# Kernel tuning notes

Hardware: AMD Instinct MI355X
Metric: run time of the kernel (lower is better)

Reference implementation:

```python
import jax, jax.numpy as jnp
import numpy as np

B, D, N, K = 16, 128, 16384, 64


def setup_inputs() -> dict:
    key = jax.random.key(0)
    k1, k2, k3, k4 = jax.random.split(key, 4)
    x = jax.random.normal(k1, (B, D, N), dtype=jnp.float32)
    mu = jax.random.normal(k2, (K, D), dtype=jnp.float32)
    log_sigma = 0.1 * jax.random.normal(k3, (K, D), dtype=jnp.float32)
    log_alpha = 0.1 * jax.random.normal(k4, (K,), dtype=jnp.float32)
    return {"x": x, "mu": mu, "log_sigma": log_sigma, "log_alpha": log_alpha}


def reference(x, mu, log_sigma, log_alpha):
    # x: (B, D, N) -> (B, N, D)
    xt = jnp.transpose(x, (0, 2, 1))
    # F.normalize(mu): L2-normalize each cluster center along D (eps=1e-12)
    mu_n = mu / jnp.maximum(jnp.linalg.norm(mu, axis=1, keepdims=True), 1e-12)
    sigma_inv = jnp.exp(-log_sigma)                     # (K, D)
    log_sigma_sum = jnp.sum(log_sigma, axis=1)          # (K,)
    # dist_{bnk} = sum_d (x-mu)^2 * sinv, decomposed into GEMMs
    xsq_term = jnp.einsum('bnd,kd->bnk', xt * xt, sigma_inv)
    cross = jnp.einsum('bnd,kd->bnk', xt, mu_n * sigma_inv)
    mu_term = jnp.sum(mu_n * mu_n * sigma_inv, axis=1)  # (K,)
    dist = xsq_term - 2.0 * cross + mu_term
    logits = -dist + log_alpha - 0.5 * log_sigma_sum    # (B, N, K)
    posterior = jax.nn.softmax(logits, axis=-1)
    return jnp.transpose(posterior, (0, 2, 1))          # (B, K, N)
```

## Files before the change

### kernel.cpp

```cpp
#include <hip/hip_runtime.h>

#define LOG2E 1.4426950408889634f

constexpr int Dn = 128;
constexpr int Nn = 16384;
constexpr int Kn = 64;
constexpr int Bn = 16;

typedef __attribute__((ext_vector_type(16))) float f32x16;

__global__ __launch_bounds__(64) void gmm_prep(const float* __restrict__ mu,
                                               const float* __restrict__ log_sigma,
                                               const float* __restrict__ log_alpha,
                                               float4* __restrict__ wout,
                                               float* __restrict__ cout) {
    const int k = blockIdx.x;
    const int l = threadIdx.x;
    const int d0 = 2 * l;
    float m0 = mu[k * Dn + d0];
    float m1 = mu[k * Dn + d0 + 1];
    float s0 = log_sigma[k * Dn + d0];
    float s1 = log_sigma[k * Dn + d0 + 1];
    float nrm2 = m0 * m0 + m1 * m1;
    float lss = s0 + s1;
    #pragma unroll
    for (int off = 32; off > 0; off >>= 1) {
        nrm2 += __shfl_xor(nrm2, off);
        lss  += __shfl_xor(lss, off);
    }
    const float inv_nrm = 1.0f / fmaxf(sqrtf(nrm2), 1e-12f);
    const float mn0 = m0 * inv_nrm, mn1 = m1 * inv_nrm;
    const float si0 = expf(-s0), si1 = expf(-s1);
    float mt = mn0 * mn0 * si0 + mn1 * mn1 * si1;
    #pragma unroll
    for (int off = 32; off > 0; off >>= 1) mt += __shfl_xor(mt, off);
    wout[((k >> 3) * 64 + l) * 8 + (k & 7)] =
        make_float4(-si0 * LOG2E, 2.0f * mn0 * si0 * LOG2E,
                    -si1 * LOG2E, 2.0f * mn1 * si1 * LOG2E);
    if (l == 0) cout[k] = (log_alpha[k] - 0.5f * lss - mt) * LOG2E;
}

__device__ __forceinline__ float4 fmax4(float4 a, float4 b) {
    return make_float4(fmaxf(a.x, b.x), fmaxf(a.y, b.y),
                       fmaxf(a.z, b.z), fmaxf(a.w, b.w));
}
__device__ __forceinline__ float4 add4(float4 a, float4 b) {
    return make_float4(a.x + b.x, a.y + b.y, a.z + b.z, a.w + b.w);
}

__global__ __launch_bounds__(512)
void gmm_main(const float* __restrict__ x,
              const float4* __restrict__ w,
              const float* __restrict__ cks,
              float* __restrict__ out) {
    __shared__ float sRed[8][256];

    const int tid = threadIdx.x;
    const int g = __builtin_amdgcn_readfirstlane(tid >> 6);
    const int l = tid & 63;
    const int b = blockIdx.y;
    const int nloc = 4 * l;
    const size_t nbase = (size_t)blockIdx.x * 256 + nloc;

    float acc[8][4];
    #pragma unroll
    for (int k = 0; k < 8; ++k) {
        const float c = cks[g * 8 + k];
        #pragma unroll
        for (int j = 0; j < 4; ++j) acc[k][j] = c;
    }

    const float* xp = x + (size_t)b * Dn * Nn + nbase;
    const char* wp = (const char*)w + (size_t)g * 8192;

    #pragma unroll 1
    for (int dh = 0; dh < Dn / 2; ++dh) {
        const float4 xa = *(const float4*)(xp);
        const float4 xb = *(const float4*)(xp + Nn);
        xp += 2 * Nn;

        f32x16 w0, w1;
        asm("s_load_dwordx16 %0, %2, 0x0\n\t"
            "s_load_dwordx16 %1, %2, 0x40\n\t"
            "s_waitcnt lgkmcnt(0)"
            : "=&s"(w0), "=&s"(w1)
            : "s"(wp));
        wp += 128;

        const float4 ta = make_float4(xa.x * xa.x, xa.y * xa.y,
                                      xa.z * xa.z, xa.w * xa.w);
        const float4 tb = make_float4(xb.x * xb.x, xb.y * xb.y,
                                      xb.z * xb.z, xb.w * xb.w);

#define GMM_K(WV, KK, A)                                                  \
        {                                                                 \
            const float wx0 = WV[4 * KK + 0], wy0 = WV[4 * KK + 1];       \
            const float wx1 = WV[4 * KK + 2], wy1 = WV[4 * KK + 3];       \
            A[0] = fmaf(wx0, ta.x, A[0]); A[0] = fmaf(wy0, xa.x, A[0]);   \
            A[0] = fmaf(wx1, tb.x, A[0]); A[0] = fmaf(wy1, xb.x, A[0]);   \
            A[1] = fmaf(wx0, ta.y, A[1]); A[1] = fmaf(wy0, xa.y, A[1]);   \
            A[1] = fmaf(wx1, tb.y, A[1]); A[1] = fmaf(wy1, xb.y, A[1]);   \
            A[2] = fmaf(wx0, ta.z, A[2]); A[2] = fmaf(wy0, xa.z, A[2]);   \
            A[2] = fmaf(wx1, tb.z, A[2]); A[2] = fmaf(wy1, xb.z, A[2]);   \
            A[3] = fmaf(wx0, ta.w, A[3]); A[3] = fmaf(wy0, xa.w, A[3]);   \
            A[3] = fmaf(wx1, tb.w, A[3]); A[3] = fmaf(wy1, xb.w, A[3]);   \
        }

        GMM_K(w0, 0, acc[0]); GMM_K(w0, 1, acc[1]);
        GMM_K(w0, 2, acc[2]); GMM_K(w0, 3, acc[3]);
        GMM_K(w1, 0, acc[4]); GMM_K(w1, 1, acc[5]);
        GMM_K(w1, 2, acc[6]); GMM_K(w1, 3, acc[7]);
#undef GMM_K
    }

    float4 m = make_float4(acc[0][0], acc[0][1], acc[0][2], acc[0][3]);
    #pragma unroll
    for (int k = 1; k < 8; ++k)
        m = fmax4(m, make_float4(acc[k][0], acc[k][1], acc[k][2], acc[k][3]));
    *(float4*)&sRed[g][nloc] = m;
    __syncthreads();
    #pragma unroll
    for (int gg = 0; gg < 8; ++gg)
        m = fmax4(m, *(const float4*)&sRed[gg][nloc]);
    __syncthreads();

    float4 s = make_float4(0.f, 0.f, 0.f, 0.f);
    #pragma unroll
    for (int k = 0; k < 8; ++k) {
        acc[k][0] = __builtin_amdgcn_exp2f(acc[k][0] - m.x); s.x += acc[k][0];
        acc[k][1] = __builtin_amdgcn_exp2f(acc[k][1] - m.y); s.y += acc[k][1];
        acc[k][2] = __builtin_amdgcn_exp2f(acc[k][2] - m.z); s.z += acc[k][2];
        acc[k][3] = __builtin_amdgcn_exp2f(acc[k][3] - m.w); s.w += acc[k][3];
    }
    *(float4*)&sRed[g][nloc] = s;
    __syncthreads();
    s = make_float4(0.f, 0.f, 0.f, 0.f);
    #pragma unroll
    for (int gg = 0; gg < 8; ++gg)
        s = add4(s, *(const float4*)&sRed[gg][nloc]);
    const float4 r = make_float4(1.0f / s.x, 1.0f / s.y, 1.0f / s.z, 1.0f / s.w);

    float* op = out + (size_t)(b * Kn + g * 8) * Nn + nbase;
    #pragma unroll
    for (int k = 0; k < 8; ++k) {
        *(float4*)op = make_float4(acc[k][0] * r.x, acc[k][1] * r.y,
                                   acc[k][2] * r.z, acc[k][3] * r.w);
        op += Nn;
    }
}

extern "C" void kernel_launch(void* const* d_in, const int* in_sizes, int n_in,
                              void* d_out, int out_size, void* d_ws, size_t ws_size,
                              hipStream_t stream) {
    const float* x  = (const float*)d_in[0];
    const float* mu = (const float*)d_in[1];
    const float* ls = (const float*)d_in[2];
    const float* la = (const float*)d_in[3];
    float* out = (float*)d_out;

    float4* wbuf = (float4*)d_ws;
    float*  cbuf = (float*)((char*)d_ws + (size_t)Kn * (Dn / 2) * sizeof(float4));

    gmm_prep<<<dim3(Kn), dim3(64), 0, stream>>>(mu, ls, la, wbuf, cbuf);
    gmm_main<<<dim3(Nn / 256, Bn), dim3(512), 0, stream>>>(x, wbuf, cbuf, out);
}
```

Before: 261.5 us.

## Split clusters across 16 waves per block and software-prefetch x rows

Each block now runs 16 waves of 64 lanes, each handling 4 clusters instead of 8, so the same 256 points are covered by twice as many waves. The weight layout in the prep kernel changes to match, and the cross-wave softmax reduction grows to 16 rows. The main loop now handles four d-rows per iteration and prefetches the next four x rows into registers while computing the current ones, using a safe dummy address on the last iteration. This aims to raise occupancy and hide global-load latency, at the cost of every wave reading x redundantly (16 times per block instead of 8) and a larger shared-memory reduction.

```diff
diff --git a/kernel.cpp b/kernel.cpp
--- a/kernel.cpp
+++ b/kernel.cpp
@@ -34,7 +34,7 @@
     float mt = mn0 * mn0 * si0 + mn1 * mn1 * si1;
     #pragma unroll
     for (int off = 32; off > 0; off >>= 1) mt += __shfl_xor(mt, off);
-    wout[((k >> 3) * 64 + l) * 8 + (k & 7)] =
+    wout[((k >> 2) * 64 + l) * 4 + (k & 3)] =
         make_float4(-si0 * LOG2E, 2.0f * mn0 * si0 * LOG2E,
                     -si1 * LOG2E, 2.0f * mn1 * si1 * LOG2E);
     if (l == 0) cout[k] = (log_alpha[k] - 0.5f * lss - mt) * LOG2E;
@@ -47,13 +47,17 @@
 __device__ __forceinline__ float4 add4(float4 a, float4 b) {
     return make_float4(a.x + b.x, a.y + b.y, a.z + b.z, a.w + b.w);
 }
+__device__ __forceinline__ float4 sq4(float4 a) {
+    return make_float4(a.x * a.x, a.y * a.y, a.z * a.z, a.w * a.w);
+}
 
-__global__ __launch_bounds__(512)
+__global__ __launch_bounds__(1024)
+__attribute__((amdgpu_waves_per_eu(8, 8)))
 void gmm_main(const float* __restrict__ x,
               const float4* __restrict__ w,
               const float* __restrict__ cks,
               float* __restrict__ out) {
-    __shared__ float sRed[8][256];
+    __shared__ float sRed[16][256];
 
     const int tid = threadIdx.x;
     const int g = __builtin_amdgcn_readfirstlane(tid >> 6);
@@ -62,23 +66,26 @@
     const int nloc = 4 * l;
     const size_t nbase = (size_t)blockIdx.x * 256 + nloc;
 
-    float acc[8][4];
+    float acc[4][4];
     #pragma unroll
-    for (int k = 0; k < 8; ++k) {
-        const float c = cks[g * 8 + k];
+    for (int k = 0; k < 4; ++k) {
+        const float c = cks[g * 4 + k];
         #pragma unroll
         for (int j = 0; j < 4; ++j) acc[k][j] = c;
     }
 
     const float* xp = x + (size_t)b * Dn * Nn + nbase;
-    const char* wp = (const char*)w + (size_t)g * 8192;
+    const float* const xsafe = xp;
+    const char* wp = (const char*)w + (size_t)g * 4096;
+
+    float4 xa0 = *(const float4*)(xp);
+    float4 xb0 = *(const float4*)(xp + Nn);
+    float4 xa1 = *(const float4*)(xp + 2 * Nn);
+    float4 xb1 = *(const float4*)(xp + 3 * Nn);
+    xp += 4 * Nn;
 
     #pragma unroll 1
-    for (int dh = 0; dh < Dn / 2; ++dh) {
-        const float4 xa = *(const float4*)(xp);
-        const float4 xb = *(const float4*)(xp + Nn);
-        xp += 2 * Nn;
-
+    for (int dh = 0; dh < Dn / 2; dh += 2) {
         f32x16 w0, w1;
         asm("s_load_dwordx16 %0, %2, 0x0\n\t"
             "s_load_dwordx16 %1, %2, 0x40\n\t"
@@ -87,46 +94,59 @@
             : "s"(wp));
         wp += 128;
 
-        const float4 ta = make_float4(xa.x * xa.x, xa.y * xa.y,
-                                      xa.z * xa.z, xa.w * xa.w);
-        const float4 tb = make_float4(xb.x * xb.x, xb.y * xb.y,
-                                      xb.z * xb.z, xb.w * xb.w);
+        const float* xq = (dh < Dn / 2 - 2) ? xp : xsafe;
+        const float4 na0 = *(const float4*)(xq);
+        const float4 nb0 = *(const float4*)(xq + Nn);
+        const float4 na1 = *(const float4*)(xq + 2 * Nn);
+        const float4 nb1 = *(const float4*)(xq + 3 * Nn);
+        xp += 4 * Nn;
 
-#define GMM_K(WV, KK, A)                                                  \
+#define GMM_K(WV, KK, A, TA, XA, TB, XB)                                  \
         {                                                                 \
             const float wx0 = WV[4 * KK + 0], wy0 = WV[4 * KK + 1];       \
             const float wx1 = WV[4 * KK + 2], wy1 = WV[4 * KK + 3];       \
-            A[0] = fmaf(wx0, ta.x, A[0]); A[0] = fmaf(wy0, xa.x, A[0]);   \
-            A[0] = fmaf(wx1, tb.x, A[0]); A[0] = fmaf(wy1, xb.x, A[0]);   \
-            A[1] = fmaf(wx0, ta.y, A[1]); A[1] = fmaf(wy0, xa.y, A[1]);   \
-            A[1] = fmaf(wx1, tb.y, A[1]); A[1] = fmaf(wy1, xb.y, A[1]);   \
-            A[2] = fmaf(wx0, ta.z, A[2]); A[2] = fmaf(wy0, xa.z, A[2]);   \
-            A[2] = fmaf(wx1, tb.z, A[2]); A[2] = fmaf(wy1, xb.z, A[2]);   \
-            A[3] = fmaf(wx0, ta.w, A[3]); A[3] = fmaf(wy0, xa.w, A[3]);   \
-            A[3] = fmaf(wx1, tb.w, A[3]); A[3] = fmaf(wy1, xb.w, A[3]);   \
+            A[0] = fmaf(wx0, TA.x, A[0]); A[0] = fmaf(wy0, XA.x, A[0]);   \
+            A[0] = fmaf(wx1, TB.x, A[0]); A[0] = fmaf(wy1, XB.x, A[0]);   \
+            A[1] = fmaf(wx0, TA.y, A[1]); A[1] = fmaf(wy0, XA.y, A[1]);   \
+            A[1] = fmaf(wx1, TB.y, A[1]); A[1] = fmaf(wy1, XB.y, A[1]);   \
+            A[2] = fmaf(wx0, TA.z, A[2]); A[2] = fmaf(wy0, XA.z, A[2]);   \
+            A[2] = fmaf(wx1, TB.z, A[2]); A[2] = fmaf(wy1, XB.z, A[2]);   \
+            A[3] = fmaf(wx0, TA.w, A[3]); A[3] = fmaf(wy0, XA.w, A[3]);   \
+            A[3] = fmaf(wx1, TB.w, A[3]); A[3] = fmaf(wy1, XB.w, A[3]);   \
         }
 
-        GMM_K(w0, 0, acc[0]); GMM_K(w0, 1, acc[1]);
-        GMM_K(w0, 2, acc[2]); GMM_K(w0, 3, acc[3]);
-        GMM_K(w1, 0, acc[4]); GMM_K(w1, 1, acc[5]);
-        GMM_K(w1, 2, acc[6]); GMM_K(w1, 3, acc[7]);
+        {
+            const float4 ta = sq4(xa0), tb = sq4(xb0);
+            GMM_K(w0, 0, acc[0], ta, xa0, tb, xb0);
+            GMM_K(w0, 1, acc[1], ta, xa0, tb, xb0);
+            GMM_K(w0, 2, acc[2], ta, xa0, tb, xb0);
+            GMM_K(w0, 3, acc[3], ta, xa0, tb, xb0);
+        }
+        {
+            const float4 ta = sq4(xa1), tb = sq4(xb1);
+            GMM_K(w1, 0, acc[0], ta, xa1, tb, xb1);
+            GMM_K(w1, 1, acc[1], ta, xa1, tb, xb1);
+            GMM_K(w1, 2, acc[2], ta, xa1, tb, xb1);
+            GMM_K(w1, 3, acc[3], ta, xa1, tb, xb1);
+        }
 #undef GMM_K
+        xa0 = na0; xb0 = nb0; xa1 = na1; xb1 = nb1;
     }
 
     float4 m = make_float4(acc[0][0], acc[0][1], acc[0][2], acc[0][3]);
     #pragma unroll
-    for (int k = 1; k < 8; ++k)
+    for (int k = 1; k < 4; ++k)
         m = fmax4(m, make_float4(acc[k][0], acc[k][1], acc[k][2], acc[k][3]));
     *(float4*)&sRed[g][nloc] = m;
     __syncthreads();
     #pragma unroll
-    for (int gg = 0; gg < 8; ++gg)
+    for (int gg = 0; gg < 16; ++gg)
         m = fmax4(m, *(const float4*)&sRed[gg][nloc]);
     __syncthreads();
 
     float4 s = make_float4(0.f, 0.f, 0.f, 0.f);
     #pragma unroll
-    for (int k = 0; k < 8; ++k) {
+    for (int k = 0; k < 4; ++k) {
         acc[k][0] = __builtin_amdgcn_exp2f(acc[k][0] - m.x); s.x += acc[k][0];
         acc[k][1] = __builtin_amdgcn_exp2f(acc[k][1] - m.y); s.y += acc[k][1];
         acc[k][2] = __builtin_amdgcn_exp2f(acc[k][2] - m.z); s.z += acc[k][2];
@@ -136,13 +156,13 @@
     __syncthreads();
     s = make_float4(0.f, 0.f, 0.f, 0.f);
     #pragma unroll
-    for (int gg = 0; gg < 8; ++gg)
+    for (int gg = 0; gg < 16; ++gg)
         s = add4(s, *(const float4*)&sRed[gg][nloc]);
     const float4 r = make_float4(1.0f / s.x, 1.0f / s.y, 1.0f / s.z, 1.0f / s.w);
 
-    float* op = out + (size_t)(b * Kn + g * 8) * Nn + nbase;
+    float* op = out + (size_t)(b * Kn + g * 4) * Nn + nbase;
     #pragma unroll
-    for (int k = 0; k < 8; ++k) {
+    for (int k = 0; k < 4; ++k) {
         *(float4*)op = make_float4(acc[k][0] * r.x, acc[k][1] * r.y,
                                    acc[k][2] * r.z, acc[k][3] * r.w);
         op += Nn;
@@ -162,5 +182,5 @@
     float*  cbuf = (float*)((char*)d_ws + (size_t)Kn * (Dn / 2) * sizeof(float4));
 
     gmm_prep<<<dim3(Kn), dim3(64), 0, stream>>>(mu, ls, la, wbuf, cbuf);
-    gmm_main<<<dim3(Nn / 256, Bn), dim3(512), 0, stream>>>(x, wbuf, cbuf, out);
+    gmm_main<<<dim3(Nn / 256, Bn), dim3(1024), 0, stream>>>(x, wbuf, cbuf, out);
 }
```

Result: no change. 265.4 us (+1.5%).

## Stage x slabs in LDS with async loads and use packed fp32 FMAs

Applied to the files above, without the earlier changes.

Before, each of the 8 waves in a block loaded the same x rows straight from global memory. Now each wave loads two rows of a 16-row slab into double-buffered shared memory with global_load_lds, and all waves read it from there. Accumulators become float2 pairs over cluster pairs, so the inner product can map to packed FMA instructions and issue half as many VALU ops. The weight buffer is rearranged so each d row holds 16 contiguous floats for the wave's 8 clusters, and the kernel is pinned to 8 waves per EU. The cost is extra block barriers per slab and more LDS per block, which may limit occupancy.

```diff
diff --git a/kernel.cpp b/kernel.cpp
--- a/kernel.cpp
+++ b/kernel.cpp
@@ -7,12 +7,15 @@
 constexpr int Kn = 64;
 constexpr int Bn = 16;
 
-typedef __attribute__((ext_vector_type(16))) float f32x16;
+typedef float v2f  __attribute__((ext_vector_type(2)));
+typedef float v16f __attribute__((ext_vector_type(16)));
+
+__device__ __forceinline__ v2f splat2(float v) { v2f r; r[0] = v; r[1] = v; return r; }
 
 __global__ __launch_bounds__(64) void gmm_prep(const float* __restrict__ mu,
                                                const float* __restrict__ log_sigma,
                                                const float* __restrict__ log_alpha,
-                                               float4* __restrict__ wout,
+                                               float* __restrict__ wout,
                                                float* __restrict__ cout) {
     const int k = blockIdx.x;
     const int l = threadIdx.x;
@@ -34,9 +37,15 @@
     float mt = mn0 * mn0 * si0 + mn1 * mn1 * si1;
     #pragma unroll
     for (int off = 32; off > 0; off >>= 1) mt += __shfl_xor(mt, off);
-    wout[((k >> 3) * 64 + l) * 8 + (k & 7)] =
-        make_float4(-si0 * LOG2E, 2.0f * mn0 * si0 * LOG2E,
-                    -si1 * LOG2E, 2.0f * mn1 * si1 * LOG2E);
+
+    const int gk = k >> 3;
+    const int p  = (k & 7) >> 1;
+    const int h  = k & 1;
+    float* wg = wout + (size_t)(gk * Dn + d0) * 16;
+    wg[p * 4 + h]          = -si0 * LOG2E;
+    wg[p * 4 + 2 + h]      = 2.0f * mn0 * si0 * LOG2E;
+    wg[16 + p * 4 + h]     = -si1 * LOG2E;
+    wg[16 + p * 4 + 2 + h] = 2.0f * mn1 * si1 * LOG2E;
     if (l == 0) cout[k] = (log_alpha[k] - 0.5f * lss - mt) * LOG2E;
 }
 
@@ -49,10 +58,13 @@
 }
 
 __global__ __launch_bounds__(512)
+__attribute__((amdgpu_waves_per_eu(8, 8)))
 void gmm_main(const float* __restrict__ x,
-              const float4* __restrict__ w,
+              const float* __restrict__ w,
               const float* __restrict__ cks,
               float* __restrict__ out) {
+    constexpr int SLAB = 16;
+    __shared__ float sX[2][SLAB][256];
     __shared__ float sRed[8][256];
 
     const int tid = threadIdx.x;
@@ -60,63 +72,80 @@
     const int l = tid & 63;
     const int b = blockIdx.y;
     const int nloc = 4 * l;
-    const size_t nbase = (size_t)blockIdx.x * 256 + nloc;
-
-    float acc[8][4];
-    #pragma unroll
-    for (int k = 0; k < 8; ++k) {
-        const float c = cks[g * 8 + k];
-        #pragma unroll
-        for (int j = 0; j < 4; ++j) acc[k][j] = c;
-    }
-
-    const float* xp = x + (size_t)b * Dn * Nn + nbase;
-    const char* wp = (const char*)w + (size_t)g * 8192;
+    const int nwin = blockIdx.x * 256;
+
+    const float* xwin = x + (size_t)b * Dn * Nn + nwin;
+
+    v2f acc[4][4];
+    #pragma unroll
+    for (int p = 0; p < 4; ++p) {
+        v2f c2; c2[0] = cks[g * 8 + 2 * p]; c2[1] = cks[g * 8 + 2 * p + 1];
+        #pragma unroll
+        for (int j = 0; j < 4; ++j) acc[j][p] = c2;
+    }
+
+    auto stage = [&](int s) {
+        #pragma unroll
+        for (int rr = 0; rr < 2; ++rr) {
+            const int r = 2 * g + rr;
+            const float* gsrc = xwin + (size_t)(s * SLAB + r) * Nn + 4 * l;
+            __builtin_amdgcn_global_load_lds(
+                (const __attribute__((address_space(1))) float*)gsrc,
+                (__attribute__((address_space(3))) float*)&sX[s & 1][r][0],
+                16, 0, 0);
+        }
+    };
+
+    stage(0);
+    const char* wp = (const char*)w + (size_t)g * (Dn * 64);
+    __syncthreads();
 
     #pragma unroll 1
-    for (int dh = 0; dh < Dn / 2; ++dh) {
-        const float4 xa = *(const float4*)(xp);
-        const float4 xb = *(const float4*)(xp + Nn);
-        xp += 2 * Nn;
-
-        f32x16 w0, w1;
-        asm("s_load_dwordx16 %0, %2, 0x0\n\t"
-            "s_load_dwordx16 %1, %2, 0x40\n\t"
-            "s_waitcnt lgkmcnt(0)"
-            : "=&s"(w0), "=&s"(w1)
-            : "s"(wp));
-        wp += 128;
-
-        const float4 ta = make_float4(xa.x * xa.x, xa.y * xa.y,
-                                      xa.z * xa.z, xa.w * xa.w);
-        const float4 tb = make_float4(xb.x * xb.x, xb.y * xb.y,
-                                      xb.z * xb.z, xb.w * xb.w);
-
-#define GMM_K(WV, KK, A)                                                  \
-        {                                                                 \
-            const float wx0 = WV[4 * KK + 0], wy0 = WV[4 * KK + 1];       \
-            const float wx1 = WV[4 * KK + 2], wy1 = WV[4 * KK + 3];       \
-            A[0] = fmaf(wx0, ta.x, A[0]); A[0] = fmaf(wy0, xa.x, A[0]);   \
-            A[0] = fmaf(wx1, tb.x, A[0]); A[0] = fmaf(wy1, xb.x, A[0]);   \
-            A[1] = fmaf(wx0, ta.y, A[1]); A[1] = fmaf(wy0, xa.y, A[1]);   \
-            A[1] = fmaf(wx1, tb.y, A[1]); A[1] = fmaf(wy1, xb.y, A[1]);   \
-            A[2] = fmaf(wx0, ta.z, A[2]); A[2] = fmaf(wy0, xa.z, A[2]);   \
-            A[2] = fmaf(wx1, tb.z, A[2]); A[2] = fmaf(wy1, xb.z, A[2]);   \
-            A[3] = fmaf(wx0, ta.w, A[3]); A[3] = fmaf(wy0, xa.w, A[3]);   \
-            A[3] = fmaf(wx1, tb.w, A[3]); A[3] = fmaf(wy1, xb.w, A[3]);   \
+    for (int s = 0; s < Dn / SLAB; ++s) {
+        if (s + 1 < Dn / SLAB) stage(s + 1);
+        const float* xs = &sX[s & 1][0][nloc];
+        #pragma unroll
+        for (int r = 0; r < SLAB; ++r) {
+            const float4 xv = *(const float4*)(xs + r * 256);
+            const v16f wv = *(const v16f*)(wp + (s * SLAB + r) * 64);
+            const float tx = xv.x * xv.x, ty = xv.y * xv.y;
+            const float tz = xv.z * xv.z, tw = xv.w * xv.w;
+            #pragma unroll
+            for (int p = 0; p < 4; ++p) {
+                v2f wa; wa[0] = wv[4 * p];     wa[1] = wv[4 * p + 1];
+                v2f wb; wb[0] = wv[4 * p + 2]; wb[1] = wv[4 * p + 3];
+                acc[0][p] = __builtin_elementwise_fma(wa, splat2(tx),   acc[0][p]);
+                acc[0][p] = __builtin_elementwise_fma(wb, splat2(xv.x), acc[0][p]);
+                acc[1][p] = __builtin_elementwise_fma(wa, splat2(ty),   acc[1][p]);
+                acc[1][p] = __builtin_elementwise_fma(wb, splat2(xv.y), acc[1][p]);
+                acc[2][p] = __builtin_elementwise_fma(wa, splat2(tz),   acc[2][p]);
+                acc[2][p] = __builtin_elementwise_fma(wb, splat2(xv.z), acc[2][p]);
+                acc[3][p] = __builtin_elementwise_fma(wa, splat2(tw),   acc[3][p]);
+                acc[3][p] = __builtin_elementwise_fma(wb, splat2(xv.w), acc[3][p]);
+            }
         }
-
-        GMM_K(w0, 0, acc[0]); GMM_K(w0, 1, acc[1]);
-        GMM_K(w0, 2, acc[2]); GMM_K(w0, 3, acc[3]);
-        GMM_K(w1, 0, acc[4]); GMM_K(w1, 1, acc[5]);
-        GMM_K(w1, 2, acc[6]); GMM_K(w1, 3, acc[7]);
-#undef GMM_K
-    }
-
-    float4 m = make_float4(acc[0][0], acc[0][1], acc[0][2], acc[0][3]);
-    #pragma unroll
-    for (int k = 1; k < 8; ++k)
-        m = fmax4(m, make_float4(acc[k][0], acc[k][1], acc[k][2], acc[k][3]));
+        __syncthreads();
+    }
+
+    float4 m;
+    {
+        #pragma unroll
+        for (int j = 0; j < 1; ++j) {}
+        v2f m20 = __builtin_elementwise_max(acc[0][0], acc[0][1]);
+        v2f q0  = __builtin_elementwise_max(acc[0][2], acc[0][3]);
+        m20 = __builtin_elementwise_max(m20, q0);
+        v2f m21 = __builtin_elementwise_max(acc[1][0], acc[1][1]);
+        v2f q1  = __builtin_elementwise_max(acc[1][2], acc[1][3]);
+        m21 = __builtin_elementwise_max(m21, q1);
+        v2f m22 = __builtin_elementwise_max(acc[2][0], acc[2][1]);
+        v2f q2  = __builtin_elementwise_max(acc[2][2], acc[2][3]);
+        m22 = __builtin_elementwise_max(m22, q2);
+        v2f m23 = __builtin_elementwise_max(acc[3][0], acc[3][1]);
+        v2f q3  = __builtin_elementwise_max(acc[3][2], acc[3][3]);
+        m23 = __builtin_elementwise_max(m23, q3);
+        m = make_float4(fmaxf(m20[0], m20[1]), fmaxf(m21[0], m21[1]),
+                        fmaxf(m22[0], m22[1]), fmaxf(m23[0], m23[1]));
+    }
     *(float4*)&sRed[g][nloc] = m;
     __syncthreads();
     #pragma unroll
@@ -124,28 +153,35 @@
         m = fmax4(m, *(const float4*)&sRed[gg][nloc]);
     __syncthreads();
 
-    float4 s = make_float4(0.f, 0.f, 0.f, 0.f);
-    #pragma unroll
-    for (int k = 0; k < 8; ++k) {
-        acc[k][0] = __builtin_amdgcn_exp2f(acc[k][0] - m.x); s.x += acc[k][0];
-        acc[k][1] = __builtin_amdgcn_exp2f(acc[k][1] - m.y); s.y += acc[k][1];
-        acc[k][2] = __builtin_amdgcn_exp2f(acc[k][2] - m.z); s.z += acc[k][2];
-        acc[k][3] = __builtin_amdgcn_exp2f(acc[k][3] - m.w); s.w += acc[k][3];
-    }
-    *(float4*)&sRed[g][nloc] = s;
-    __syncthreads();
-    s = make_float4(0.f, 0.f, 0.f, 0.f);
+    float4 s4 = make_float4(0.f, 0.f, 0.f, 0.f);
+    #pragma unroll
+    for (int p = 0; p < 4; ++p) {
+        acc[0][p][0] = __builtin_amdgcn_exp2f(acc[0][p][0] - m.x); s4.x += acc[0][p][0];
+        acc[0][p][1] = __builtin_amdgcn_exp2f(acc[0][p][1] - m.x); s4.x += acc[0][p][1];
+        acc[1][p][0] = __builtin_amdgcn_exp2f(acc[1][p][0] - m.y); s4.y += acc[1][p][0];
+        acc[1][p][1] = __builtin_amdgcn_exp2f(acc[1][p][1] - m.y); s4.y += acc[1][p][1];
+        acc[2][p][0] = __builtin_amdgcn_exp2f(acc[2][p][0] - m.z); s4.z += acc[2][p][0];
+        acc[2][p][1] = __builtin_amdgcn_exp2f(acc[2][p][1] - m.z); s4.z += acc[2][p][1];
+        acc[3][p][0] = __builtin_amdgcn_exp2f(acc[3][p][0] - m.w); s4.w += acc[3][p][0];
+        acc[3][p][1] = __builtin_amdgcn_exp2f(acc[3][p][1] - m.w); s4.w += acc[3][p][1];
+    }
+    *(float4*)&sRed[g][nloc] = s4;
+    __syncthreads();
+    s4 = make_float4(0.f, 0.f, 0.f, 0.f);
     #pragma unroll
     for (int gg = 0; gg < 8; ++gg)
-        s = add4(s, *(const float4*)&sRed[gg][nloc]);
-    const float4 r = make_float4(1.0f / s.x, 1.0f / s.y, 1.0f / s.z, 1.0f / s.w);
-
-    float* op = out + (size_t)(b * Kn + g * 8) * Nn + nbase;
-    #pragma unroll
-    for (int k = 0; k < 8; ++k) {
-        *(float4*)op = make_float4(acc[k][0] * r.x, acc[k][1] * r.y,
-                                   acc[k][2] * r.z, acc[k][3] * r.w);
-        op += Nn;
+        s4 = add4(s4, *(const float4*)&sRed[gg][nloc]);
+    const float4 r4 = make_float4(1.0f / s4.x, 1.0f / s4.y, 1.0f / s4.z, 1.0f / s4.w);
+
+    float* op = out + (size_t)(b * Kn + g * 8) * Nn + nwin + nloc;
+    #pragma unroll
+    for (int p = 0; p < 4; ++p) {
+        #pragma unroll
+        for (int h = 0; h < 2; ++h) {
+            *(float4*)op = make_float4(acc[0][p][h] * r4.x, acc[1][p][h] * r4.y,
+                                       acc[2][p][h] * r4.z, acc[3][p][h] * r4.w);
+            op += Nn;
+        }
     }
 }
 
@@ -158,8 +194,8 @@
     const float* la = (const float*)d_in[3];
     float* out = (float*)d_out;
 
-    float4* wbuf = (float4*)d_ws;
-    float*  cbuf = (float*)((char*)d_ws + (size_t)Kn * (Dn / 2) * sizeof(float4));
+    float* wbuf = (float*)d_ws;
+    float* cbuf = (float*)((char*)d_ws + (size_t)8 * Dn * 16 * sizeof(float));
 
     gmm_prep<<<dim3(Kn), dim3(64), 0, stream>>>(mu, ls, la, wbuf, cbuf);
     gmm_main<<<dim3(Nn / 256, Bn), dim3(512), 0, stream>>>(x, wbuf, cbuf, out);
```

Measured after the change: 264.7 us. No clear change (+1.2%).

## Use packed FP32 FMA with 16-cluster groups and two-column thread tiles

Applied to the files above, without the earlier changes.

Moves the inner product onto v_pk_fma_f32, where each instruction updates two cluster accumulators for one column using a packed scalar weight pair. The weight layout is rebuilt into 16-cluster groups so each wave loads 256 bytes of SGPR weights per step. Each wave now owns 16 clusters by 2 columns instead of 8 clusters by 4 columns. The aim is to halve VALU issue count in the FMA-bound loop. In exchange, x loads become 8-byte, output stores become float2, and scalar load traffic per FLOP doubles.

```diff
diff --git a/kernel.cpp b/kernel.cpp
--- a/kernel.cpp
+++ b/kernel.cpp
@@ -7,12 +7,13 @@
 constexpr int Kn = 64;
 constexpr int Bn = 16;
 
+typedef float v2f __attribute__((ext_vector_type(2)));
 typedef __attribute__((ext_vector_type(16))) float f32x16;
 
 __global__ __launch_bounds__(64) void gmm_prep(const float* __restrict__ mu,
                                                const float* __restrict__ log_sigma,
                                                const float* __restrict__ log_alpha,
-                                               float4* __restrict__ wout,
+                                               float* __restrict__ wout,
                                                float* __restrict__ cout) {
     const int k = blockIdx.x;
     const int l = threadIdx.x;
@@ -34,117 +35,132 @@
     float mt = mn0 * mn0 * si0 + mn1 * mn1 * si1;
     #pragma unroll
     for (int off = 32; off > 0; off >>= 1) mt += __shfl_xor(mt, off);
-    wout[((k >> 3) * 64 + l) * 8 + (k & 7)] =
-        make_float4(-si0 * LOG2E, 2.0f * mn0 * si0 * LOG2E,
-                    -si1 * LOG2E, 2.0f * mn1 * si1 * LOG2E);
+
+    const int kg = k >> 4;
+    const int p  = (k & 15) >> 1;
+    const int h  = k & 1;
+    float* rec = wout + ((size_t)kg * Dn + d0) * 32;
+    rec[4 * p + h]          = -si0 * LOG2E;
+    rec[4 * p + 2 + h]      = 2.0f * mn0 * si0 * LOG2E;
+    rec[32 + 4 * p + h]     = -si1 * LOG2E;
+    rec[32 + 4 * p + 2 + h] = 2.0f * mn1 * si1 * LOG2E;
     if (l == 0) cout[k] = (log_alpha[k] - 0.5f * lss - mt) * LOG2E;
-}
-
-__device__ __forceinline__ float4 fmax4(float4 a, float4 b) {
-    return make_float4(fmaxf(a.x, b.x), fmaxf(a.y, b.y),
-                       fmaxf(a.z, b.z), fmaxf(a.w, b.w));
-}
-__device__ __forceinline__ float4 add4(float4 a, float4 b) {
-    return make_float4(a.x + b.x, a.y + b.y, a.z + b.z, a.w + b.w);
 }
 
 __global__ __launch_bounds__(512)
 void gmm_main(const float* __restrict__ x,
-              const float4* __restrict__ w,
+              const float* __restrict__ w,
               const float* __restrict__ cks,
               float* __restrict__ out) {
-    __shared__ float sRed[8][256];
+    __shared__ float sRed[4][256];
 
     const int tid = threadIdx.x;
     const int g = __builtin_amdgcn_readfirstlane(tid >> 6);
+    const int kg = g & 3;
+    const int nh = g >> 2;
     const int l = tid & 63;
     const int b = blockIdx.y;
-    const int nloc = 4 * l;
+    const int nloc = nh * 128 + 2 * l;
     const size_t nbase = (size_t)blockIdx.x * 256 + nloc;
 
-    float acc[8][4];
+    v2f acc[8][2];
     #pragma unroll
-    for (int k = 0; k < 8; ++k) {
-        const float c = cks[g * 8 + k];
-        #pragma unroll
-        for (int j = 0; j < 4; ++j) acc[k][j] = c;
+    for (int p = 0; p < 8; ++p) {
+        v2f c; c[0] = cks[kg * 16 + 2 * p]; c[1] = cks[kg * 16 + 2 * p + 1];
+        acc[p][0] = c; acc[p][1] = c;
     }
 
     const float* xp = x + (size_t)b * Dn * Nn + nbase;
-    const char* wp = (const char*)w + (size_t)g * 8192;
+    const char* wp = (const char*)w + (size_t)kg * (Dn * 32 * 4);
+
+#define PK_FMA_LO(A, W, X)                                                   \
+    asm("v_pk_fma_f32 %0, %2, %1, %0 op_sel:[0,0,0] op_sel_hi:[1,0,1]"       \
+        : "+v"(A) : "v"(X), "s"(W))
+#define PK_FMA_HI(A, W, X)                                                   \
+    asm("v_pk_fma_f32 %0, %2, %1, %0 op_sel:[0,1,0] op_sel_hi:[1,1,1]"       \
+        : "+v"(A) : "v"(X), "s"(W))
+#define GMM_P(WV, Q, T, X, AP)                                               \
+    {                                                                        \
+        v2f wa; wa[0] = WV[4 * (Q)];     wa[1] = WV[4 * (Q) + 1];            \
+        v2f wb; wb[0] = WV[4 * (Q) + 2]; wb[1] = WV[4 * (Q) + 3];            \
+        PK_FMA_LO(AP[0], wa, T); PK_FMA_LO(AP[0], wb, X);                    \
+        PK_FMA_HI(AP[1], wa, T); PK_FMA_HI(AP[1], wb, X);                    \
+    }
 
     #pragma unroll 1
-    for (int dh = 0; dh < Dn / 2; ++dh) {
-        const float4 xa = *(const float4*)(xp);
-        const float4 xb = *(const float4*)(xp + Nn);
+    for (int it = 0; it < Dn / 2; ++it) {
+        const v2f x0 = *(const v2f*)(xp);
+        const v2f x1 = *(const v2f*)(xp + Nn);
         xp += 2 * Nn;
 
-        f32x16 w0, w1;
-        asm("s_load_dwordx16 %0, %2, 0x0\n\t"
-            "s_load_dwordx16 %1, %2, 0x40\n\t"
-            "s_waitcnt lgkmcnt(0)"
-            : "=&s"(w0), "=&s"(w1)
-            : "s"(wp));
-        wp += 128;
+        f32x16 w0, w1, w2, w3;
+        asm volatile("s_load_dwordx16 %0, %4, 0x0\n\t"
+                     "s_load_dwordx16 %1, %4, 0x40\n\t"
+                     "s_load_dwordx16 %2, %4, 0x80\n\t"
+                     "s_load_dwordx16 %3, %4, 0xC0\n\t"
+                     "s_waitcnt lgkmcnt(0)"
+                     : "=&s"(w0), "=&s"(w1), "=&s"(w2), "=&s"(w3)
+                     : "s"(wp));
+        wp += 256;
 
-        const float4 ta = make_float4(xa.x * xa.x, xa.y * xa.y,
-                                      xa.z * xa.z, xa.w * xa.w);
-        const float4 tb = make_float4(xb.x * xb.x, xb.y * xb.y,
-                                      xb.z * xb.z, xb.w * xb.w);
+        const v2f t0 = x0 * x0;
+        const v2f t1 = x1 * x1;
 
-#define GMM_K(WV, KK, A)                                                  \
-        {                                                                 \
-            const float wx0 = WV[4 * KK + 0], wy0 = WV[4 * KK + 1];       \
-            const float wx1 = WV[4 * KK + 2], wy1 = WV[4 * KK + 3];       \
-            A[0] = fmaf(wx0, ta.x, A[0]); A[0] = fmaf(wy0, xa.x, A[0]);   \
-            A[0] = fmaf(wx1, tb.x, A[0]); A[0] = fmaf(wy1, xb.x, A[0]);   \
-            A[1] = fmaf(wx0, ta.y, A[1]); A[1] = fmaf(wy0, xa.y, A[1]);   \
-            A[1] = fmaf(wx1, tb.y, A[1]); A[1] = fmaf(wy1, xb.y, A[1]);   \
-            A[2] = fmaf(wx0, ta.z, A[2]); A[2] = fmaf(wy0, xa.z, A[2]);   \
-            A[2] = fmaf(wx1, tb.z, A[2]); A[2] = fmaf(wy1, xb.z, A[2]);   \
-            A[3] = fmaf(wx0, ta.w, A[3]); A[3] = fmaf(wy0, xa.w, A[3]);   \
-            A[3] = fmaf(wx1, tb.w, A[3]); A[3] = fmaf(wy1, xb.w, A[3]);   \
-        }
+        GMM_P(w0, 0, t0, x0, acc[0]); GMM_P(w0, 1, t0, x0, acc[1]);
+        GMM_P(w0, 2, t0, x0, acc[2]); GMM_P(w0, 3, t0, x0, acc[3]);
+        GMM_P(w1, 0, t0, x0, acc[4]); GMM_P(w1, 1, t0, x0, acc[5]);
+        GMM_P(w1, 2, t0, x0, acc[6]); GMM_P(w1, 3, t0, x0, acc[7]);
 
-        GMM_K(w0, 0, acc[0]); GMM_K(w0, 1, acc[1]);
-        GMM_K(w0, 2, acc[2]); GMM_K(w0, 3, acc[3]);
-        GMM_K(w1, 0, acc[4]); GMM_K(w1, 1, acc[5]);
-        GMM_K(w1, 2, acc[6]); GMM_K(w1, 3, acc[7]);
-#undef GMM_K
+        GMM_P(w2, 0, t1, x1, acc[0]); GMM_P(w2, 1, t1, x1, acc[1]);
+        GMM_P(w2, 2, t1, x1, acc[2]); GMM_P(w2, 3, t1, x1, acc[3]);
+        GMM_P(w3, 0, t1, x1, acc[4]); GMM_P(w3, 1, t1, x1, acc[5]);
+        GMM_P(w3, 2, t1, x1, acc[6]); GMM_P(w3, 3, t1, x1, acc[7]);
     }
+#undef GMM_P
+#undef PK_FMA_LO
+#undef PK_FMA_HI
 
-    float4 m = make_float4(acc[0][0], acc[0][1], acc[0][2], acc[0][3]);
+    v2f mx0 = acc[0][0], mx1 = acc[0][1];
     #pragma unroll
-    for (int k = 1; k < 8; ++k)
-        m = fmax4(m, make_float4(acc[k][0], acc[k][1], acc[k][2], acc[k][3]));
-    *(float4*)&sRed[g][nloc] = m;
+    for (int p = 1; p < 8; ++p) {
+        mx0 = __builtin_elementwise_max(mx0, acc[p][0]);
+        mx1 = __builtin_elementwise_max(mx1, acc[p][1]);
+    }
+    float m0 = fmaxf(mx0[0], mx0[1]);
+    float m1 = fmaxf(mx1[0], mx1[1]);
+    *(float2*)&sRed[kg][nloc] = make_float2(m0, m1);
     __syncthreads();
     #pragma unroll
-    for (int gg = 0; gg < 8; ++gg)
-        m = fmax4(m, *(const float4*)&sRed[gg][nloc]);
+    for (int q = 0; q < 4; ++q) {
+        const float2 mm = *(const float2*)&sRed[q][nloc];
+        m0 = fmaxf(m0, mm.x); m1 = fmaxf(m1, mm.y);
+    }
     __syncthreads();
 
-    float4 s = make_float4(0.f, 0.f, 0.f, 0.f);
+    float s0 = 0.f, s1 = 0.f;
     #pragma unroll
-    for (int k = 0; k < 8; ++k) {
-        acc[k][0] = __builtin_amdgcn_exp2f(acc[k][0] - m.x); s.x += acc[k][0];
-        acc[k][1] = __builtin_amdgcn_exp2f(acc[k][1] - m.y); s.y += acc[k][1];
-        acc[k][2] = __builtin_amdgcn_exp2f(acc[k][2] - m.z); s.z += acc[k][2];
-        acc[k][3] = __builtin_amdgcn_exp2f(acc[k][3] - m.w); s.w += acc[k][3];
+    for (int p = 0; p < 8; ++p) {
+        acc[p][0][0] = __builtin_amdgcn_exp2f(acc[p][0][0] - m0); s0 += acc[p][0][0];
+        acc[p][0][1] = __builtin_amdgcn_exp2f(acc[p][0][1] - m0); s0 += acc[p][0][1];
+        acc[p][1][0] = __builtin_amdgcn_exp2f(acc[p][1][0] - m1); s1 += acc[p][1][0];
+        acc[p][1][1] = __builtin_amdgcn_exp2f(acc[p][1][1] - m1); s1 += acc[p][1][1];
     }
-    *(float4*)&sRed[g][nloc] = s;
+    *(float2*)&sRed[kg][nloc] = make_float2(s0, s1);
     __syncthreads();
-    s = make_float4(0.f, 0.f, 0.f, 0.f);
+    s0 = 0.f; s1 = 0.f;
     #pragma unroll
-    for (int gg = 0; gg < 8; ++gg)
-        s = add4(s, *(const float4*)&sRed[gg][nloc]);
-    const float4 r = make_float4(1.0f / s.x, 1.0f / s.y, 1.0f / s.z, 1.0f / s.w);
+    for (int q = 0; q < 4; ++q) {
+        const float2 ss = *(const float2*)&sRed[q][nloc];
+        s0 += ss.x; s1 += ss.y;
+    }
+    const float r0 = 1.0f / s0, r1 = 1.0f / s1;
 
-    float* op = out + (size_t)(b * Kn + g * 8) * Nn + nbase;
+    float* op = out + (size_t)(b * Kn + kg * 16) * Nn + nbase;
     #pragma unroll
-    for (int k = 0; k < 8; ++k) {
-        *(float4*)op = make_float4(acc[k][0] * r.x, acc[k][1] * r.y,
-                                   acc[k][2] * r.z, acc[k][3] * r.w);
+    for (int p = 0; p < 8; ++p) {
+        *(float2*)op = make_float2(acc[p][0][0] * r0, acc[p][1][0] * r1);
+        op += Nn;
+        *(float2*)op = make_float2(acc[p][0][1] * r0, acc[p][1][1] * r1);
         op += Nn;
     }
 }
@@ -158,8 +174,8 @@
     const float* la = (const float*)d_in[3];
     float* out = (float*)d_out;
 
-    float4* wbuf = (float4*)d_ws;
-    float*  cbuf = (float*)((char*)d_ws + (size_t)Kn * (Dn / 2) * sizeof(float4));
+    float* wbuf = (float*)d_ws;
+    float* cbuf = (float*)((char*)d_ws + (size_t)4 * Dn * 32 * sizeof(float));
 
     gmm_prep<<<dim3(Kn), dim3(64), 0, stream>>>(mu, ls, la, wbuf, cbuf);
     gmm_main<<<dim3(Nn / 256, Bn), dim3(512), 0, stream>>>(x, wbuf, cbuf, out);
```

Result: slower. 270.1 us (+3.3%).
